# Performance work log

Hardware: AMD Instinct MI355X
Metric: run time of the kernel (lower is better)

Reference implementation:

```python
import jax, jax.numpy as jnp
import numpy as np
from jax import lax

B, CIN, COUT, N, H, W = 8, 64, 64, 9, 128, 128
KS, PAD = 3, 1
EPS = 1e-5
DN = ('NCHW', 'OIHW', 'NCHW')

def _conv(x, w, b, pad):
    y = lax.conv_general_dilated(x, w, (1, 1), [(pad, pad), (pad, pad)], dimension_numbers=DN)
    return y + b[None, :, None, None]

def setup_inputs() -> dict:
    key = jax.random.key(0)
    ks = jax.random.split(key, 8)
    fan = CIN * KS * KS
    s = 1.0 / np.sqrt(fan)
    return {
        'x': jax.random.normal(ks[0], (B, CIN, H, W), dtype=jnp.float32),
        'kernels_w': jax.random.uniform(ks[1], (N, COUT, CIN, KS, KS), minval=-s, maxval=s, dtype=jnp.float32),
        'kernels_b': jax.random.uniform(ks[2], (N, COUT), minval=-s, maxval=s, dtype=jnp.float32),
        'obs1_w': jax.random.uniform(ks[3], (COUT // 2, CIN, 1, 1), minval=-1/np.sqrt(CIN), maxval=1/np.sqrt(CIN), dtype=jnp.float32),
        'obs1_b': jax.random.uniform(ks[4], (COUT // 2,), minval=-1/np.sqrt(CIN), maxval=1/np.sqrt(CIN), dtype=jnp.float32),
        'obs2_w': jax.random.uniform(ks[5], (N, COUT // 2, 1, 1), minval=-1/np.sqrt(COUT // 2), maxval=1/np.sqrt(COUT // 2), dtype=jnp.float32),
        'obs2_b': jax.random.uniform(ks[6], (N,), minval=-1/np.sqrt(COUT // 2), maxval=1/np.sqrt(COUT // 2), dtype=jnp.float32),
        'gamma': jnp.ones((COUT,), dtype=jnp.float32),
        'beta': jnp.zeros((COUT,), dtype=jnp.float32),
    }

def reference(x, kernels_w, kernels_b, obs1_w, obs1_b, obs2_w, obs2_b, gamma, beta):
    b, _, h, w = x.shape
    # all N path convs as one grouped-output conv: (B, N*COUT, H, W)
    paths = _conv(x, kernels_w.reshape(N * COUT, CIN, KS, KS), kernels_b.reshape(-1), PAD)
    paths = paths.reshape(b, N, COUT, h, w)
    # observer: 1x1 conv -> tanh -> 1x1 conv, scores (B, N, H, W)
    scores = _conv(jnp.tanh(_conv(x, obs1_w, obs1_b, 0)), obs2_w, obs2_b, 0)
    # eval-mode collapse: per-pixel argmax over paths, one-hot weighted sum == gather
    idx = jnp.argmax(scores, axis=1)  # (B, H, W)
    sel = jnp.take_along_axis(paths, idx[:, None, None, :, :], axis=1)[:, 0]  # (B, COUT, H, W)
    out = jax.nn.relu(sel)
    # ModularPhaseNorm2d (assumed instance-norm-style per-channel spatial norm with affine)
    mu = jnp.mean(out, axis=(2, 3), keepdims=True)
    var = jnp.var(out, axis=(2, 3), keepdims=True)
    y = (out - mu) * lax.rsqrt(var + EPS)
    return y * gamma[None, :, None, None] + beta[None, :, None, None]
```

## Files before the change

kernel.cpp:

```cpp
#include <hip/hip_runtime.h>
#include <hip/hip_bf16.h>
#include <stdint.h>

#define B_    8
#define CIN   64
#define COUT  64
#define NPATH 9
#define H_    128
#define W_    128
#define HW    16384
#define PTOT  131072
#define NBIN  72
#define CHUNK 64
#define NBLK  256
#define NSCORE 1024
#define PMASK 0x1FFFFu

typedef float  f32x4   __attribute__((ext_vector_type(4)));
typedef float  f32x16  __attribute__((ext_vector_type(16)));
typedef __bf16 bf16x8  __attribute__((ext_vector_type(8)));
typedef short  short8  __attribute__((ext_vector_type(8)));
typedef unsigned short ushort4v __attribute__((ext_vector_type(4)));

__device__ __forceinline__ short f2bf(float f) {
    __bf16 b = (__bf16)f;
    return __builtin_bit_cast(short, b);
}
__device__ __forceinline__ float bf2f(unsigned short u) {
    unsigned v = ((unsigned)u) << 16;
    return __builtin_bit_cast(float, v);
}
__device__ __forceinline__ float fast_tanh(float a) {
    float e = __builtin_amdgcn_exp2f(a * 2.885390081777927f);
    return 1.0f - 2.0f / (e + 1.0f);
}

#define GC(arr, i)  ((arr)[(i) * 16])
#define SM(arr, i)  ((arr)[(i) * 16])

__global__ void k_zero(f32x4* __restrict__ dst) {
    int i = blockIdx.x * 256 + threadIdx.x;
    if (i < 5120) dst[i] = (f32x4)0.0f;
}

__global__ __launch_bounds__(256, 2) void k_pre(
                      const float* __restrict__ x,
                      const float* __restrict__ w1, const float* __restrict__ b1,
                      const float* __restrict__ w2, const float* __restrict__ b2,
                      const float* __restrict__ kw,
                      unsigned* __restrict__ gcnt, unsigned* __restrict__ lists,
                      unsigned short* __restrict__ Xbg,
                      unsigned short* __restrict__ WbF) {
    int t = threadIdx.x;
    if (blockIdx.x >= NSCORE) {
        int ob = ((int)blockIdx.x - NSCORE) * 4096 + t * 16;
        #pragma unroll
        for (int j = 0; j < 16; ++j) {
            int o = ob + j;
            int jj   = o & 7;
            int lane = (o >> 3) & 63;
            int f    = (o >> 9) & 3;
            int rest = o >> 11;
            int s    = rest % 18;
            int n    = rest / 18;
            int c    = f * 16 + (lane & 15);
            int kg   = lane >> 4;
            int ci   = ((s & 1) << 5) + (kg << 3) + jj;
            int tap  = s >> 1;
            WbF[o] = (unsigned short)f2bf(kw[((n * 64 + c) * 64 + ci) * 9 + tap]);
        }
        return;
    }
    __shared__ float xt[64 * 128];
    __shared__ float ht[32 * 128];
    __shared__ float w1t[64 * 36];
    __shared__ float w2s[304];
    __shared__ unsigned scnt[NBIN];
    __shared__ unsigned sbase[NBIN];

    int px0 = blockIdx.x * 128;
    int b   = blockIdx.x >> 7;
    int hw0 = px0 & 16383;
    if (t < NBIN) scnt[t] = 0u;

    const float* xbp = x + (((size_t)b) << 20) + hw0;
    #pragma unroll
    for (int i = 0; i < 8; ++i) {
        int flat = i * 256 + t;
        int ch = flat >> 5, ck = flat & 31;
        f32x4 v = *(const f32x4*)(xbp + ch * HW + ck * 4);
        *(f32x4*)(&xt[ch * 128 + ck * 4]) = v;
    }
    #pragma unroll
    for (int i = 0; i < 8; ++i) {
        int flat = i * 256 + t;
        int j = flat >> 6, ch = flat & 63;
        w1t[ch * 36 + j] = w1[flat];
    }
    for (int i = t; i < 288; i += 256) w2s[i] = w2[i];
    if (t < 9) w2s[288 + t] = b2[t];
    __syncthreads();

    int wv = t >> 6, l = t & 63;
    {
        float acc[8][2];
        #pragma unroll
        for (int jj = 0; jj < 8; ++jj) {
            float bj = b1[wv * 8 + jj];
            acc[jj][0] = bj; acc[jj][1] = bj;
        }
        #pragma unroll 8
        for (int ch = 0; ch < 64; ++ch) {
            f32x4 wa = *(const f32x4*)(&w1t[ch * 36 + wv * 8]);
            f32x4 wb = *(const f32x4*)(&w1t[ch * 36 + wv * 8 + 4]);
            float2 xx = *(const float2*)(&xt[ch * 128 + l * 2]);
            #pragma unroll
            for (int jj = 0; jj < 4; ++jj) {
                acc[jj][0]     += xx.x * wa[jj];
                acc[jj][1]     += xx.y * wa[jj];
                acc[4 + jj][0] += xx.x * wb[jj];
                acc[4 + jj][1] += xx.y * wb[jj];
            }
        }
        #pragma unroll
        for (int jj = 0; jj < 8; ++jj)
            *(float2*)(&ht[(wv * 8 + jj) * 128 + l * 2]) =
                make_float2(acc[jj][0], acc[jj][1]);
    }
    __syncthreads();

    int bin = 0; unsigned rank = 0, entry = 0;
    if (t < 128) {
        int px = t;
        float h[32];
        #pragma unroll
        for (int j = 0; j < 32; ++j) h[j] = fast_tanh(ht[j * 128 + px]);
        float best = -1e30f; int bi = 0;
        #pragma unroll
        for (int nn = 0; nn < 9; ++nn) {
            float a = w2s[288 + nn];
            #pragma unroll
            for (int i = 0; i < 16; ++i)
                a += h[i] * w2s[nn * 32 + i] + h[16 + i] * w2s[nn * 32 + 16 + i];
            if (a > best) { best = a; bi = nn; }
        }
        bin = bi * 8 + b;
        int p = px0 + px;
        int hh = (p >> 7) & 127, ww = p & 127;
        unsigned m = 0;
        #pragma unroll
        for (int tap = 0; tap < 9; ++tap) {
            int dh = tap / 3 - 1, dw = tap % 3 - 1;
            if ((unsigned)(hh + dh) < 128u && (unsigned)(ww + dw) < 128u) m |= (1u << tap);
        }
        entry = (unsigned)p | (m << 23);
        rank = atomicAdd(&scnt[bin], 1u);
    } else {
        int px = t - 128;
        size_t xo = ((size_t)(px0 + px)) << 6;
        #pragma unroll
        for (int v8 = 0; v8 < 8; ++v8) {
            short8 pk;
            #pragma unroll
            for (int i = 0; i < 8; ++i)
                pk[i] = f2bf(xt[(v8 * 8 + i) * 128 + px]);
            *(short8*)(Xbg + xo + v8 * 8) = pk;
        }
    }
    __syncthreads();
    if (t < NBIN && scnt[t]) sbase[t] = atomicAdd(&GC(gcnt, t), scnt[t]);
    __syncthreads();
    if (t < 128) lists[bin * 16384 + sbase[bin] + rank] = entry;
}

__global__ __launch_bounds__(512, 2) void k_conv(
        const unsigned short* __restrict__ Xbg, const unsigned short* __restrict__ WbF,
        const float* __restrict__ kb, const unsigned* __restrict__ lists,
        const unsigned* __restrict__ gcnt,
        unsigned short* __restrict__ Yc, float* __restrict__ sums) {
    __shared__ char blds[2][73728];
    __shared__ unsigned sgc[NBIN];
    __shared__ unsigned sst[NBIN + 1];
    int t = threadIdx.x;
    int wid = t >> 6, lane = t & 63, kg = lane >> 4, l15 = lane & 15;
    int f = wid & 3, gh = wid >> 2;
    int spx = t >> 3, q = t & 7;
    int sq8 = (q ^ (spx & 7)) * 8;
    int dst16 = t * 16;

    if (t < NBIN) sgc[t] = GC(gcnt, t);
    __syncthreads();
    if (t == 0) {
        unsigned acc = 0;
        for (int bin = 0; bin < NBIN; ++bin) {
            sst[bin] = acc;
            acc += (sgc[bin] + (CHUNK - 1u)) / CHUNK;
        }
        sst[NBIN] = acc;
    }
    __syncthreads();
    unsigned C = sst[NBIN];

    #define CINFO(K, BIN, CNT, BAS) do {                          \
        int lo_ = 0, hi_ = NBIN;                                  \
        _Pragma("unroll")                                         \
        for (int it_ = 0; it_ < 7; ++it_) {                       \
            if (hi_ - lo_ > 1) {                                  \
                int mid_ = (lo_ + hi_) >> 1;                      \
                if (sst[mid_] <= (K)) lo_ = mid_; else hi_ = mid_;\
            }                                                     \
        }                                                         \
        BIN = lo_;                                                \
        CNT = (int)sgc[lo_];                                      \
        BAS = (int)((K) - sst[lo_]) * CHUNK;                      \
    } while (0)

    unsigned bid = (blockIdx.x & 7) * 32 + (blockIdx.x >> 3);
    unsigned c0 = (bid * C) / NBLK, c1 = ((bid + 1) * C) / NBLK;
    if (c0 >= c1) return;

    short8 g[9];
    #define GLOAD(E) do {                                                         \
        int pp_ = (int)((E) & PMASK);                                             \
        const unsigned short* bp_ = Xbg + ((size_t)pp_ << 6) + sq8;               \
        g[0] = *(const short8*)(bp_ - 129 * 64);                                  \
        g[1] = *(const short8*)(bp_ - 128 * 64);                                  \
        g[2] = *(const short8*)(bp_ - 127 * 64);                                  \
        g[3] = *(const short8*)(bp_ -   1 * 64);                                  \
        g[4] = *(const short8*)(bp_);                                             \
        g[5] = *(const short8*)(bp_ +   1 * 64);                                  \
        g[6] = *(const short8*)(bp_ + 127 * 64);                                  \
        g[7] = *(const short8*)(bp_ + 128 * 64);                                  \
        g[8] = *(const short8*)(bp_ + 129 * 64);                                  \
    } while (0)

    int cb, cc_, cbase;
    CINFO(c0, cb, cc_, cbase);
    unsigned cps  = lists[cb * 16384 + min(cbase + spx,            cc_ - 1)];
    unsigned cpm0 = lists[cb * 16384 + min(cbase + gh * 32 + l15,      cc_ - 1)];
    unsigned cpm1 = lists[cb * 16384 + min(cbase + gh * 32 + 16 + l15, cc_ - 1)];
    GLOAD(cps);

    int nb, nc_, nbase;
    {
        unsigned k1 = min(c0 + 1, c1 - 1);
        CINFO(k1, nb, nc_, nbase);
    }
    unsigned nps  = lists[nb * 16384 + min(nbase + spx,            nc_ - 1)];
    unsigned npm0 = lists[nb * 16384 + min(nbase + gh * 32 + l15,      nc_ - 1)];
    unsigned npm1 = lists[nb * 16384 + min(nbase + gh * 32 + 16 + l15, nc_ - 1)];

    int n = cb >> 3, b = cb & 7;
    short8 wv[18];
    #pragma unroll
    for (int s = 0; s < 18; ++s)
        wv[s] = *(const short8*)(WbF + n * 36864 + ((s * 4 + f) * 64 + lane) * 8);
    f32x4 bias = *(const f32x4*)(kb + n * 64 + f * 16 + kg * 4);

    asm volatile("s_waitcnt vmcnt(0)" ::: "memory");
    #pragma unroll
    for (int k = 0; k < 9; ++k) *(short8*)(&blds[0][k * 8192 + dst16]) = g[k];
    asm volatile("s_waitcnt lgkmcnt(0)" ::: "memory");

    int cur = 0;
    float s1[4] = {0.f,0.f,0.f,0.f}, s2[4] = {0.f,0.f,0.f,0.f};

    for (unsigned c = c0; c < c1; ++c) {
        __builtin_amdgcn_s_barrier();
        GLOAD(nps);

        int v0 = (cbase + gh * 32 + l15)      < cc_ ? 1 : 0;
        int v1 = (cbase + gh * 32 + 16 + l15) < cc_ ? 1 : 0;
        int inb0 = v0 ? (int)(cpm0 >> 23) : 0;
        int inb1 = v1 ? (int)(cpm1 >> 23) : 0;
        f32x4 acc0 = (f32x4)0.0f, acc1 = (f32x4)0.0f;
        const short8 zero8 = (short8)0;
        const char* bufc = blds[cur];
        int pxa = gh * 32 + l15, pxb = pxa + 16;
        #pragma unroll
        for (int s = 0; s < 18; ++s) {
            const int tap = s >> 1;
            const int pr = ((s & 1) << 2) | kg;
            bf16x8 af = __builtin_bit_cast(bf16x8, wv[s]);
            short8 ra = *(const short8*)(bufc + tap * 8192 + pxa * 128 + ((pr ^ (pxa & 7)) << 4));
            short8 rb = *(const short8*)(bufc + tap * 8192 + pxb * 128 + ((pr ^ (pxb & 7)) << 4));
            short8 sa = ((inb0 >> tap) & 1) ? ra : zero8;
            short8 sb = ((inb1 >> tap) & 1) ? rb : zero8;
            acc0 = __builtin_amdgcn_mfma_f32_16x16x32_bf16(af, __builtin_bit_cast(bf16x8, sa), acc0, 0, 0, 0);
            acc1 = __builtin_amdgcn_mfma_f32_16x16x32_bf16(af, __builtin_bit_cast(bf16x8, sb), acc1, 0, 0, 0);
        }
        {
            f32x4 o0, o1;
            #pragma unroll
            for (int r = 0; r < 4; ++r) {
                o0[r] = fmaxf(acc0[r] + bias[r], 0.0f);
                o1[r] = fmaxf(acc1[r] + bias[r], 0.0f);
            }
            if (v0) {
                ushort4v u;
                #pragma unroll
                for (int r = 0; r < 4; ++r) u[r] = (unsigned short)f2bf(o0[r]);
                *(ushort4v*)(Yc + (((size_t)(cpm0 & PMASK)) << 6) + f * 16 + kg * 4) = u;
            }
            if (v1) {
                ushort4v u;
                #pragma unroll
                for (int r = 0; r < 4; ++r) u[r] = (unsigned short)f2bf(o1[r]);
                *(ushort4v*)(Yc + (((size_t)(cpm1 & PMASK)) << 6) + f * 16 + kg * 4) = u;
            }
            #pragma unroll
            for (int r = 0; r < 4; ++r) {
                float a = v0 ? o0[r] : 0.0f, bb = v1 ? o1[r] : 0.0f;
                s1[r] += a + bb;
                s2[r] += a * a + bb * bb;
            }
        }

        int fb, fc2, fbase;
        {
            unsigned k2 = min(c + 2, c1 - 1);
            CINFO(k2, fb, fc2, fbase);
        }
        unsigned fps  = lists[fb * 16384 + min(fbase + spx,            fc2 - 1)];
        unsigned fpm0 = lists[fb * 16384 + min(fbase + gh * 32 + l15,      fc2 - 1)];
        unsigned fpm1 = lists[fb * 16384 + min(fbase + gh * 32 + 16 + l15, fc2 - 1)];

        asm volatile("s_waitcnt vmcnt(3)" ::: "memory");
        __builtin_amdgcn_sched_barrier(0);
        #pragma unroll
        for (int k = 0; k < 9; ++k) *(short8*)(&blds[cur ^ 1][k * 8192 + dst16]) = g[k];
        asm volatile("s_waitcnt lgkmcnt(0)" ::: "memory");
        __builtin_amdgcn_sched_barrier(0);

        if (nb != cb && c + 1 < c1) {
            float f1[4], f2[4];
            #pragma unroll
            for (int r = 0; r < 4; ++r) { f1[r] = s1[r]; f2[r] = s2[r]; s1[r] = 0.f; s2[r] = 0.f; }
            #pragma unroll
            for (int m = 1; m < 16; m <<= 1) {
                #pragma unroll
                for (int r = 0; r < 4; ++r) {
                    f1[r] += __shfl_xor(f1[r], m, 64);
                    f2[r] += __shfl_xor(f2[r], m, 64);
                }
            }
            if (l15 == 0) {
                #pragma unroll
                for (int r = 0; r < 4; ++r) {
                    int ch = f * 16 + kg * 4 + r;
                    atomicAdd(&SM(sums, b * 64 + ch),       f1[r]);
                    atomicAdd(&SM(sums, 512 + b * 64 + ch), f2[r]);
                }
            }
            n = nb >> 3; b = nb & 7;
            #pragma unroll
            for (int s = 0; s < 18; ++s)
                wv[s] = *(const short8*)(WbF + n * 36864 + ((s * 4 + f) * 64 + lane) * 8);
            bias = *(const f32x4*)(kb + n * 64 + f * 16 + kg * 4);
        }

        cb = nb; cc_ = nc_; cbase = nbase; cpm0 = npm0; cpm1 = npm1;
        nb = fb; nc_ = fc2; nbase = fbase; nps = fps; npm0 = fpm0; npm1 = fpm1;
        cur ^= 1;
    }

    #pragma unroll
    for (int m = 1; m < 16; m <<= 1) {
        #pragma unroll
        for (int r = 0; r < 4; ++r) {
            s1[r] += __shfl_xor(s1[r], m, 64);
            s2[r] += __shfl_xor(s2[r], m, 64);
        }
    }
    if (l15 == 0) {
        #pragma unroll
        for (int r = 0; r < 4; ++r) {
            int ch = f * 16 + kg * 4 + r;
            atomicAdd(&SM(sums, b * 64 + ch),       s1[r]);
            atomicAdd(&SM(sums, 512 + b * 64 + ch), s2[r]);
        }
    }
    #undef GLOAD
    #undef CINFO
}

__global__ void k_final(const unsigned short* __restrict__ Yc, const float* __restrict__ sums,
                        const float* __restrict__ gamma, const float* __restrict__ beta,
                        float* __restrict__ out) {
    __shared__ float ld[128][66];
    __shared__ float smu[64], srs[64], sg[64], sb[64];
    int t = threadIdx.x;
    int b = blockIdx.y, hw0 = blockIdx.x * 128;
    if (t < 64) {
        float mu = SM(sums, b * 64 + t) * (1.0f / HW);
        float vr = SM(sums, 512 + b * 64 + t) * (1.0f / HW) - mu * mu;
        smu[t] = mu;
        srs[t] = rsqrtf(fmaxf(vr, 0.0f) + 1e-5f);
        sg[t] = gamma[t]; sb[t] = beta[t];
    }
    int i = t >> 1, half = t & 1;
    const short8* row = (const short8*)(Yc + (((size_t)(b * HW + hw0 + i)) << 6) + half * 32);
    #pragma unroll
    for (int q = 0; q < 4; ++q) {
        short8 v = row[q];
        #pragma unroll
        for (int j = 0; j < 8; ++j)
            ld[i][half * 32 + q * 8 + j] = bf2f((unsigned short)v[j]);
    }
    __syncthreads();
    #pragma unroll
    for (int rep = 0; rep < 32; ++rep) {
        int idx = rep * 256 + t;
        int c = idx >> 7, j = idx & 127;
        float v = (ld[j][c] - smu[c]) * srs[c] * sg[c] + sb[c];
        out[(((size_t)b * 64 + c) << 14) + hw0 + j] = v;
    }
}

extern "C" void kernel_launch(void* const* d_in, const int* in_sizes, int n_in,
                              void* d_out, int out_size, void* d_ws, size_t ws_size,
                              hipStream_t stream) {
    const float* x    = (const float*)d_in[0];
    const float* kw   = (const float*)d_in[1];
    const float* kb   = (const float*)d_in[2];
    const float* w1   = (const float*)d_in[3];
    const float* b1   = (const float*)d_in[4];
    const float* w2   = (const float*)d_in[5];
    const float* b2   = (const float*)d_in[6];
    const float* gam  = (const float*)d_in[7];
    const float* bet  = (const float*)d_in[8];
    float* out = (float*)d_out;

    char* ws = (char*)d_ws;
    unsigned* gcnt      = (unsigned*)(ws + 0);
    float*    sums      = (float*)   (ws + 16384);
    unsigned* lists     = (unsigned*)(ws + 131072);
    unsigned short* Yc  = (unsigned short*)(ws + 5242880);
    unsigned short* Xbg = (unsigned short*)(ws + 22020096) + 8256;
    unsigned short* WbF = (unsigned short*)(ws + 38862848);

    k_zero<<<20, 256, 0, stream>>>((f32x4*)ws);
    k_pre<<<NSCORE + 81, 256, 0, stream>>>(x, w1, b1, w2, b2, kw, gcnt, lists, Xbg, WbF);
    k_conv<<<NBLK, 512, 0, stream>>>(Xbg, WbF, kb, lists, gcnt, Yc, sums);
    k_final<<<dim3(128, 8), 256, 0, stream>>>(Yc, sums, gam, bet, out);
}
```

Measured before the change: 79.40 us.

## Load conv input taps directly from global memory instead of LDS staging

Removes the double-buffered LDS staging of the 9 neighbour taps in the gathered conv kernel. Each lane now loads its MFMA B-operand fragments straight from global memory (relying on L1/L2 caching) and drops the barriers and LDS writes and reads. This cuts LDS traffic and block synchronisation and frees 144KB of LDS, which may allow more occupancy. The cost is that the four waves sharing pixels load redundantly, loads are less coalesced, and there is no prefetch overlap, so global latency is exposed within each iteration.

New measurement: 122.5 us. 1.54x slower.

```diff
diff --git a/kernel.cpp b/kernel.cpp
--- a/kernel.cpp
+++ b/kernel.cpp
@@ -178,15 +178,11 @@
         const float* __restrict__ kb, const unsigned* __restrict__ lists,
         const unsigned* __restrict__ gcnt,
         unsigned short* __restrict__ Yc, float* __restrict__ sums) {
-    __shared__ char blds[2][73728];
     __shared__ unsigned sgc[NBIN];
     __shared__ unsigned sst[NBIN + 1];
     int t = threadIdx.x;
     int wid = t >> 6, lane = t & 63, kg = lane >> 4, l15 = lane & 15;
     int f = wid & 3, gh = wid >> 2;
-    int spx = t >> 3, q = t & 7;
-    int sq8 = (q ^ (spx & 7)) * 8;
-    int dst16 = t * 16;
 
     if (t < NBIN) sgc[t] = GC(gcnt, t);
     __syncthreads();
@@ -219,34 +215,19 @@
     unsigned c0 = (bid * C) / NBLK, c1 = ((bid + 1) * C) / NBLK;
     if (c0 >= c1) return;
 
-    short8 g[9];
-    #define GLOAD(E) do {                                                         \
-        int pp_ = (int)((E) & PMASK);                                             \
-        const unsigned short* bp_ = Xbg + ((size_t)pp_ << 6) + sq8;               \
-        g[0] = *(const short8*)(bp_ - 129 * 64);                                  \
-        g[1] = *(const short8*)(bp_ - 128 * 64);                                  \
-        g[2] = *(const short8*)(bp_ - 127 * 64);                                  \
-        g[3] = *(const short8*)(bp_ -   1 * 64);                                  \
-        g[4] = *(const short8*)(bp_);                                             \
-        g[5] = *(const short8*)(bp_ +   1 * 64);                                  \
-        g[6] = *(const short8*)(bp_ + 127 * 64);                                  \
-        g[7] = *(const short8*)(bp_ + 128 * 64);                                  \
-        g[8] = *(const short8*)(bp_ + 129 * 64);                                  \
-    } while (0)
+    const int doff[9] = { -129*64, -128*64, -127*64, -1*64, 0, 1*64,
+                           127*64,  128*64,  129*64 };
 
     int cb, cc_, cbase;
     CINFO(c0, cb, cc_, cbase);
-    unsigned cps  = lists[cb * 16384 + min(cbase + spx,            cc_ - 1)];
     unsigned cpm0 = lists[cb * 16384 + min(cbase + gh * 32 + l15,      cc_ - 1)];
     unsigned cpm1 = lists[cb * 16384 + min(cbase + gh * 32 + 16 + l15, cc_ - 1)];
-    GLOAD(cps);
 
     int nb, nc_, nbase;
     {
         unsigned k1 = min(c0 + 1, c1 - 1);
         CINFO(k1, nb, nc_, nbase);
     }
-    unsigned nps  = lists[nb * 16384 + min(nbase + spx,            nc_ - 1)];
     unsigned npm0 = lists[nb * 16384 + min(nbase + gh * 32 + l15,      nc_ - 1)];
     unsigned npm1 = lists[nb * 16384 + min(nbase + gh * 32 + 16 + l15, nc_ - 1)];
 
@@ -257,38 +238,59 @@
         wv[s] = *(const short8*)(WbF + n * 36864 + ((s * 4 + f) * 64 + lane) * 8);
     f32x4 bias = *(const f32x4*)(kb + n * 64 + f * 16 + kg * 4);
 
-    asm volatile("s_waitcnt vmcnt(0)" ::: "memory");
-    #pragma unroll
-    for (int k = 0; k < 9; ++k) *(short8*)(&blds[0][k * 8192 + dst16]) = g[k];
-    asm volatile("s_waitcnt lgkmcnt(0)" ::: "memory");
-
-    int cur = 0;
     float s1[4] = {0.f,0.f,0.f,0.f}, s2[4] = {0.f,0.f,0.f,0.f};
 
     for (unsigned c = c0; c < c1; ++c) {
-        __builtin_amdgcn_s_barrier();
-        GLOAD(nps);
+        int fb, fc2, fbase;
+        {
+            unsigned k2 = min(c + 2, c1 - 1);
+            CINFO(k2, fb, fc2, fbase);
+        }
+        unsigned fpm0 = lists[fb * 16384 + min(fbase + gh * 32 + l15,      fc2 - 1)];
+        unsigned fpm1 = lists[fb * 16384 + min(fbase + gh * 32 + 16 + l15, fc2 - 1)];
 
         int v0 = (cbase + gh * 32 + l15)      < cc_ ? 1 : 0;
         int v1 = (cbase + gh * 32 + 16 + l15) < cc_ ? 1 : 0;
         int inb0 = v0 ? (int)(cpm0 >> 23) : 0;
         int inb1 = v1 ? (int)(cpm1 >> 23) : 0;
+        const unsigned short* base0 = Xbg + (((size_t)(cpm0 & PMASK)) << 6) + (kg << 3);
+        const unsigned short* base1 = Xbg + (((size_t)(cpm1 & PMASK)) << 6) + (kg << 3);
         f32x4 acc0 = (f32x4)0.0f, acc1 = (f32x4)0.0f;
         const short8 zero8 = (short8)0;
-        const char* bufc = blds[cur];
-        int pxa = gh * 32 + l15, pxb = pxa + 16;
-        #pragma unroll
-        for (int s = 0; s < 18; ++s) {
-            const int tap = s >> 1;
-            const int pr = ((s & 1) << 2) | kg;
-            bf16x8 af = __builtin_bit_cast(bf16x8, wv[s]);
-            short8 ra = *(const short8*)(bufc + tap * 8192 + pxa * 128 + ((pr ^ (pxa & 7)) << 4));
-            short8 rb = *(const short8*)(bufc + tap * 8192 + pxb * 128 + ((pr ^ (pxb & 7)) << 4));
-            short8 sa = ((inb0 >> tap) & 1) ? ra : zero8;
-            short8 sb = ((inb1 >> tap) & 1) ? rb : zero8;
-            acc0 = __builtin_amdgcn_mfma_f32_16x16x32_bf16(af, __builtin_bit_cast(bf16x8, sa), acc0, 0, 0, 0);
-            acc1 = __builtin_amdgcn_mfma_f32_16x16x32_bf16(af, __builtin_bit_cast(bf16x8, sb), acc1, 0, 0, 0);
-        }
+
+        {
+            short8 g[18];
+            #pragma unroll
+            for (int tap = 0; tap < 9; ++tap) {
+                g[tap * 2 + 0] = *(const short8*)(base0 + doff[tap]);
+                g[tap * 2 + 1] = *(const short8*)(base0 + doff[tap] + 32);
+            }
+            __builtin_amdgcn_sched_barrier(0);
+            #pragma unroll
+            for (int s = 0; s < 18; ++s) {
+                short8 sel = ((inb0 >> (s >> 1)) & 1) ? g[s] : zero8;
+                acc0 = __builtin_amdgcn_mfma_f32_16x16x32_bf16(
+                           __builtin_bit_cast(bf16x8, wv[s]),
+                           __builtin_bit_cast(bf16x8, sel), acc0, 0, 0, 0);
+            }
+        }
+        {
+            short8 g[18];
+            #pragma unroll
+            for (int tap = 0; tap < 9; ++tap) {
+                g[tap * 2 + 0] = *(const short8*)(base1 + doff[tap]);
+                g[tap * 2 + 1] = *(const short8*)(base1 + doff[tap] + 32);
+            }
+            __builtin_amdgcn_sched_barrier(0);
+            #pragma unroll
+            for (int s = 0; s < 18; ++s) {
+                short8 sel = ((inb1 >> (s >> 1)) & 1) ? g[s] : zero8;
+                acc1 = __builtin_amdgcn_mfma_f32_16x16x32_bf16(
+                           __builtin_bit_cast(bf16x8, wv[s]),
+                           __builtin_bit_cast(bf16x8, sel), acc1, 0, 0, 0);
+            }
+        }
+
         {
             f32x4 o0, o1;
             #pragma unroll
@@ -315,22 +317,6 @@
                 s2[r] += a * a + bb * bb;
             }
         }
-
-        int fb, fc2, fbase;
-        {
-            unsigned k2 = min(c + 2, c1 - 1);
-            CINFO(k2, fb, fc2, fbase);
-        }
-        unsigned fps  = lists[fb * 16384 + min(fbase + spx,            fc2 - 1)];
-        unsigned fpm0 = lists[fb * 16384 + min(fbase + gh * 32 + l15,      fc2 - 1)];
-        unsigned fpm1 = lists[fb * 16384 + min(fbase + gh * 32 + 16 + l15, fc2 - 1)];
-
-        asm volatile("s_waitcnt vmcnt(3)" ::: "memory");
-        __builtin_amdgcn_sched_barrier(0);
-        #pragma unroll
-        for (int k = 0; k < 9; ++k) *(short8*)(&blds[cur ^ 1][k * 8192 + dst16]) = g[k];
-        asm volatile("s_waitcnt lgkmcnt(0)" ::: "memory");
-        __builtin_amdgcn_sched_barrier(0);
 
         if (nb != cb && c + 1 < c1) {
             float f1[4], f2[4];
@@ -360,8 +346,7 @@
         }
 
         cb = nb; cc_ = nc_; cbase = nbase; cpm0 = npm0; cpm1 = npm1;
-        nb = fb; nc_ = fc2; nbase = fbase; nps = fps; npm0 = fpm0; npm1 = fpm1;
-        cur ^= 1;
+        nb = fb; nc_ = fc2; nbase = fbase; npm0 = fpm0; npm1 = fpm1;
     }
 
     #pragma unroll
@@ -380,7 +365,6 @@
             atomicAdd(&SM(sums, 512 + b * 64 + ch), s2[r]);
         }
     }
-    #undef GLOAD
     #undef CINFO
 }
 
```
